# Optimization experiments

Hardware: AMD Instinct MI355X
Metric: run time of the kernel (lower is better)

## Reference

```python
import jax, jax.numpy as jnp
import numpy as np

HEADS, KV_HEADS, HEAD_DIM = 32, 8, 64


def apply_rope(x, cos, sin):
    # x: [b,h,s,d], cos/sin: [s, d//2]; pairs are interleaved (even/odd)
    c = cos[None, None, :, :]
    s = sin[None, None, :, :]
    x1 = x[..., 0::2]
    x2 = x[..., 1::2]
    xn = x1 * c - x2 * s
    yn = x1 * s + x2 * c
    return jnp.stack([xn, yn], axis=-1).reshape(x.shape)


def setup_inputs() -> dict:
    key = jax.random.key(0)
    ks = jax.random.split(key, 7)
    b, s, h = 1, 2048, 2048
    return {
        "x": jax.random.normal(ks[0], (b, s, h), jnp.float32),
        "cos": jax.random.normal(ks[1], (s, HEAD_DIM // 2), jnp.float32),
        "sin": jax.random.normal(ks[2], (s, HEAD_DIM // 2), jnp.float32),
        "Wq": jax.random.normal(ks[3], (h, HEADS * HEAD_DIM), jnp.float32) * 0.02,
        "Wk": jax.random.normal(ks[4], (h, KV_HEADS * HEAD_DIM), jnp.float32) * 0.02,
        "Wv": jax.random.normal(ks[5], (h, KV_HEADS * HEAD_DIM), jnp.float32) * 0.02,
        "Wo": jax.random.normal(ks[6], (HEADS * HEAD_DIM, h), jnp.float32) * 0.02,
    }


def reference(x, cos, sin, Wq, Wk, Wv, Wo):
    b, seq, hidden = x.shape
    Q = x @ Wq  # [b,s,H*d]
    K = x @ Wk  # [b,s,Kh*d]
    V = x @ Wv
    q = Q.reshape(b, seq, HEADS, HEAD_DIM).transpose(0, 2, 1, 3)      # b h s d
    k = K.reshape(b, seq, KV_HEADS, HEAD_DIM).transpose(0, 2, 1, 3)   # b k s d
    v = V.reshape(b, seq, KV_HEADS, HEAD_DIM).transpose(0, 2, 1, 3)
    r = HEADS // KV_HEADS
    # einops 'b k s d -> b (r k) s d': tile kv-head block r times
    k = jnp.tile(k, (1, r, 1, 1))
    v = jnp.tile(v, (1, r, 1, 1))
    q = apply_rope(q, cos, sin)
    k = apply_rope(k, cos, sin)
    scale = 1.0 / jnp.sqrt(jnp.float32(HEAD_DIM))
    qk = jnp.einsum('bhqd,bhkd->bhqk', q, k) * scale
    mask = jnp.triu(jnp.full((seq, seq), -jnp.inf, qk.dtype), k=1)
    attn = jax.nn.softmax(qk + mask, axis=-1)
    av = jnp.einsum('bhqk,bhkd->bhqd', attn, v)
    av = av.transpose(0, 2, 1, 3).reshape(b, seq, HEADS * HEAD_DIM)
    return av @ Wo
```

## Files before the change

### kernel.cpp

```cpp
#include <hip/hip_runtime.h>

typedef unsigned short u16;
typedef __attribute__((ext_vector_type(4))) float f32x4;
typedef __attribute__((ext_vector_type(16))) float f32x16;
typedef __attribute__((ext_vector_type(8))) __bf16 bf16x8;
typedef __attribute__((ext_vector_type(2))) __bf16 bf16x2;

#define HEADS 32
#define KV_HEADS 8
#define HD 64
#define SEQ 2048
#define HID 2048
#define NQK 3072
#define QSCALE (0.125f * 1.4426950408889634f)
#define OCH 2097152u

#define AS1 __attribute__((address_space(1)))
#define AS3 __attribute__((address_space(3)))

__device__ __forceinline__ u16 f2bf(float f) {
  unsigned u = __float_as_uint(f);
  u += 0x7FFFu + ((u >> 16) & 1u);
  return (u16)(u >> 16);
}

__device__ __forceinline__ unsigned pk2(float a, float b) {
  union { bf16x2 h; unsigned u; } c;
  c.h[0] = (__bf16)a; c.h[1] = (__bf16)b;
  return c.u;
}

__device__ __forceinline__ float bflo(unsigned u) {
  return __uint_as_float(u << 16);
}
__device__ __forceinline__ float bfhi(unsigned u) {
  return __uint_as_float(u & 0xFFFF0000u);
}

__device__ __forceinline__ void load16_to_lds(const void* g, void* l) {
  __builtin_amdgcn_global_load_lds((AS1 void*)(void*)g, (AS3 void*)l, 16, 0, 0);
}

__global__ __launch_bounds__(256) void k_f2b(const float* __restrict__ in,
                                             u16* __restrict__ out, int n4) {
  int i = blockIdx.x * 256 + threadIdx.x;
  if (i >= n4) return;
  float4 v = ((const float4*)in)[i];
  ushort4 o;
  o.x = f2bf(v.x); o.y = f2bf(v.y); o.z = f2bf(v.z); o.w = f2bf(v.w);
  ((ushort4*)out)[i] = o;
}

__global__ __launch_bounds__(256) void k_tconv(const float* __restrict__ in, int ldi,
                                               u16* __restrict__ out, int ldo) {
  __shared__ float tile[32][33];
  int c0 = blockIdx.x * 32, r0 = blockIdx.y * 32;
  int col = threadIdx.x & 31, rw = threadIdx.x >> 5;
#pragma unroll
  for (int i = 0; i < 4; i++)
    tile[rw + i * 8][col] = in[(size_t)(r0 + rw + i * 8) * ldi + c0 + col];
  __syncthreads();
#pragma unroll
  for (int i = 0; i < 4; i++)
    out[(size_t)(c0 + rw + i * 8) * ldo + r0 + col] = f2bf(tile[col][rw + i * 8]);
}


__device__ __forceinline__ void stage3(const u16* Asrc, const u16* Bsrc0,
                                       const u16* Bsrc1, u16* AsX, u16* BsX,
                                       int tid) {
  load16_to_lds(Asrc, AsX + tid * 8);
  load16_to_lds(Bsrc0, BsX + tid * 8);
  load16_to_lds(Bsrc1, BsX + 2048 + tid * 8);
}

__device__ __forceinline__ void frag_mfma(const u16* Asb, const u16* Bsb,
                                          const int* aoff, const int* boff,
                                          f32x4 acc[2][4]) {
  bf16x8 a[2], b[4];
#pragma unroll
  for (int i = 0; i < 2; i++)
    a[i] = *(const bf16x8*)((const char*)Asb + aoff[i]);
#pragma unroll
  for (int j = 0; j < 4; j++)
    b[j] = *(const bf16x8*)((const char*)Bsb + boff[j]);
#pragma unroll
  for (int i = 0; i < 2; i++)
#pragma unroll
    for (int j = 0; j < 4; j++)
      acc[i][j] = __builtin_amdgcn_mfma_f32_16x16x32_bf16(a[i], b[j], acc[i][j], 0, 0, 0);
}

__global__ __launch_bounds__(256) void k_gemm(const u16* __restrict__ A,
                                              const u16* __restrict__ Bt,
                                              float* __restrict__ C,
                                              int M, int N, int K) {
  __shared__ u16 As0[64 * 32], As1[64 * 32];
  __shared__ u16 Bs0[128 * 32], Bs1[128 * 32];
  int tid = threadIdx.x;
  int m0 = blockIdx.x * 64, n0 = blockIdx.y * 128;
  int l = tid & 63, w = tid >> 6;
  int lr = l & 15, lg = l >> 4;
  int wr = (w >> 1) * 32, wc = (w & 1) * 64;
  f32x4 acc[2][4] = {};

  int srow = tid >> 2;
  int sseg = (tid & 3) ^ ((srow >> 1) & 3);
  const u16* Asrc = A + (size_t)(m0 + srow) * K + sseg * 8;
  const u16* Bsrc0 = Bt + (size_t)(n0 + srow) * K + sseg * 8;
  const u16* Bsrc1 = Bt + (size_t)(n0 + 64 + srow) * K + sseg * 8;

  int aoff[2], boff[4];
#pragma unroll
  for (int i = 0; i < 2; i++) {
    int r = wr + i * 16 + lr;
    aoff[i] = r * 64 + ((lg ^ ((r >> 1) & 3)) << 4);
  }
#pragma unroll
  for (int j = 0; j < 4; j++) {
    int r = wc + j * 16 + lr;
    boff[j] = r * 64 + ((lg ^ ((r >> 1) & 3)) << 4);
  }

  stage3(Asrc, Bsrc0, Bsrc1, As0, Bs0, tid);
  __syncthreads();
  for (int k0 = 0; k0 < K; k0 += 64) {
    stage3(Asrc + k0 + 32, Bsrc0 + k0 + 32, Bsrc1 + k0 + 32, As1, Bs1, tid);
    frag_mfma(As0, Bs0, aoff, boff, acc);
    __syncthreads();
    if (k0 + 64 < K)
      stage3(Asrc + k0 + 64, Bsrc0 + k0 + 64, Bsrc1 + k0 + 64, As0, Bs0, tid);
    frag_mfma(As1, Bs1, aoff, boff, acc);
    __syncthreads();
  }

#pragma unroll
  for (int i = 0; i < 2; i++)
#pragma unroll
    for (int j = 0; j < 4; j++)
#pragma unroll
      for (int r = 0; r < 4; r++)
        C[(size_t)(m0 + wr + i * 16 + lg * 4 + r) * N + n0 + wc + j * 16 + lr] =
            acc[i][j][r];
}

__global__ __launch_bounds__(256) void k_gemm_qkv(const u16* __restrict__ A,
                                                  const u16* __restrict__ Bt,
                                                  const float* __restrict__ cosp,
                                                  const float* __restrict__ sinp,
                                                  u16* __restrict__ qbuf,
                                                  u16* __restrict__ kbuf,
                                                  u16* __restrict__ vtb) {
  __shared__ u16 As0[64 * 32], As1[64 * 32];
  __shared__ u16 Bs0[128 * 32], Bs1[128 * 32];
  __shared__ u16 Ts[128 * 64];
  const int K = HID;
  int tid = threadIdx.x;
  int m0 = blockIdx.x * 64, n0 = blockIdx.y * 128;
  int l = tid & 63, w = tid >> 6;
  int lr = l & 15, lg = l >> 4;
  int wr = (w >> 1) * 32, wc = (w & 1) * 64;
  f32x4 acc[2][4] = {};

  int srow = tid >> 2;
  int sseg = (tid & 3) ^ ((srow >> 1) & 3);
  const u16* Asrc = A + (size_t)(m0 + srow) * K + sseg * 8;
  const u16* Bsrc0 = Bt + (size_t)(n0 + srow) * K + sseg * 8;
  const u16* Bsrc1 = Bt + (size_t)(n0 + 64 + srow) * K + sseg * 8;

  int aoff[2], boff[4];
#pragma unroll
  for (int i = 0; i < 2; i++) {
    int r = wr + i * 16 + lr;
    aoff[i] = r * 64 + ((lg ^ ((r >> 1) & 3)) << 4);
  }
#pragma unroll
  for (int j = 0; j < 4; j++) {
    int r = wc + j * 16 + lr;
    boff[j] = r * 64 + ((lg ^ ((r >> 1) & 3)) << 4);
  }

  stage3(Asrc, Bsrc0, Bsrc1, As0, Bs0, tid);
  __syncthreads();
  for (int k0 = 0; k0 < K; k0 += 64) {
    stage3(Asrc + k0 + 32, Bsrc0 + k0 + 32, Bsrc1 + k0 + 32, As1, Bs1, tid);
    frag_mfma(As0, Bs0, aoff, boff, acc);
    __syncthreads();
    if (k0 + 64 < K)
      stage3(Asrc + k0 + 64, Bsrc0 + k0 + 64, Bsrc1 + k0 + 64, As0, Bs0, tid);
    frag_mfma(As1, Bs1, aoff, boff, acc);
    __syncthreads();
  }

  if (n0 < 2560) {
    int colbase = n0 + wc;
    bool isQ = colbase < 2048;
    float scale = isQ ? QSCALE : 1.0f;
    u16* base = isQ ? qbuf + (size_t)(colbase >> 6) * SEQ * HD
                    : kbuf + (size_t)((colbase - 2048) >> 6) * SEQ * HD;
    int odd = lr & 1;
#pragma unroll
    for (int i = 0; i < 2; i++)
#pragma unroll
      for (int j = 0; j < 4; j++) {
        int ii = j * 8 + (lr >> 1);
#pragma unroll
        for (int r = 0; r < 4; r++) {
          float v = acc[i][j][r];
          float vp = __shfl_xor(v, 1, 64);
          int sr = m0 + wr + i * 16 + lg * 4 + r;
          float cs = cosp[sr * 32 + ii], sn = sinp[sr * 32 + ii];
          float x1 = odd ? vp : v, x2 = odd ? v : vp;
          float o = odd ? (x1 * sn + x2 * cs) : (x1 * cs - x2 * sn);
          base[(size_t)sr * HD + j * 16 + lr] = f2bf(o * scale);
        }
      }
  } else {
#pragma unroll
    for (int i = 0; i < 2; i++)
#pragma unroll
      for (int j = 0; j < 4; j++)
#pragma unroll
        for (int r = 0; r < 4; r++) {
          int cB = wc + j * 16 + lr, rB = wr + i * 16 + lg * 4 + r;
          *(u16*)((char*)Ts + cB * 128 + ((rB * 2) ^ ((cB & 7) << 4))) =
              f2bf(acc[i][j][r]);
        }
    __syncthreads();
    int c = tid >> 1, half = tid & 1;
    int col = n0 + c;
    int kvh = (col - 2560) >> 6, d = col & 63;
    u16* dst = vtb + (size_t)kvh * HD * SEQ + (size_t)d * SEQ + m0 + half * 32;
    const char* src = (const char*)Ts + c * 128;
    int cs7 = (c & 7) << 4;
#pragma unroll
    for (int q = 0; q < 4; q++)
      *(uint4*)(dst + q * 8) = *(const uint4*)(src + ((half * 64 + q * 16) ^ cs7));
  }
}

__global__ __launch_bounds__(256) void k_flash2(const u16* __restrict__ qb,
                                                const u16* __restrict__ kb,
                                                const u16* __restrict__ vt,
                                                unsigned* __restrict__ Opart,
                                                float2* __restrict__ ml) {
  __shared__ u16 Ks[2][64 * 64];
  __shared__ u16 Vs[2][64 * 64];
  int bid = blockIdx.x;
  int c = bid & 1;
  int b5 = bid >> 1;
  int h = b5 & 31;
  int qi = b5 >> 5;
  int qblk = (SEQ / 128) - 1 - qi;
  int kvh = h & 7;
  int tid = threadIdx.x, w = tid >> 6, l = tid & 63;
  int lq = l & 31, hi = l >> 5;
  const u16* qh = qb + (size_t)h * SEQ * HD;
  const u16* kh = kb + (size_t)kvh * SEQ * HD;
  const u16* vh = vt + (size_t)kvh * HD * SEQ;
  int wq0 = qblk * 128 + w * 32;
  int qg = wq0 + lq;

  bf16x8 qf[4];
#pragma unroll
  for (int ds = 0; ds < 4; ds++)
    qf[ds] = *(const bf16x8*)(qh + (size_t)qg * HD + ds * 16 + hi * 8);

  f32x16 acc[2] = {};
  float m_r = -__builtin_inff(), l_r = 0.f;

  int srow = tid >> 2, c4 = tid & 3, swz = (srow & 7) << 4;
  int sd0 = srow * 128 + ((c4 * 32) ^ swz);
  int sd1 = srow * 128 + ((c4 * 32 + 16) ^ swz);
  const int kt0 = c * (qblk + 1), kt1 = kt0 + qblk + 1;

  {
    const u16* ksrc = kh + (size_t)(kt0 * 64 + srow) * HD + c4 * 16;
    const u16* vsrc = vh + (size_t)srow * SEQ + kt0 * 64 + c4 * 16;
    uint4 a0 = *(const uint4*)(ksrc), a1 = *(const uint4*)(ksrc + 8);
    uint4 b0 = *(const uint4*)(vsrc), b1 = *(const uint4*)(vsrc + 8);
    *(uint4*)((char*)Ks[0] + sd0) = a0; *(uint4*)((char*)Ks[0] + sd1) = a1;
    *(uint4*)((char*)Vs[0] + sd0) = b0; *(uint4*)((char*)Vs[0] + sd1) = b1;
  }
  __syncthreads();

  uint4 kr0, kr1, vr0, vr1;
  int lswz = (lq & 7) << 4;
  for (int kt = kt0; kt < kt1; kt++) {
    int b = (kt - kt0) & 1;
    if (kt + 1 < kt1) {
      const u16* ksrc = kh + (size_t)((kt + 1) * 64 + srow) * HD + c4 * 16;
      const u16* vsrc = vh + (size_t)srow * SEQ + (kt + 1) * 64 + c4 * 16;
      kr0 = *(const uint4*)(ksrc); kr1 = *(const uint4*)(ksrc + 8);
      vr0 = *(const uint4*)(vsrc); vr1 = *(const uint4*)(vsrc + 8);
    }

    if (kt * 64 <= wq0 + 31) {
      f32x16 sT[2] = {};
      const char* kbase = (const char*)Ks[b];
      __builtin_amdgcn_s_setprio(1);
#pragma unroll
      for (int t = 0; t < 2; t++) {
#pragma unroll
        for (int ds = 0; ds < 4; ds++) {
          bf16x8 kf = *(const bf16x8*)(kbase + (t * 32 + lq) * 128 +
                                       ((ds * 32 + hi * 16) ^ lswz));
          sT[t] = __builtin_amdgcn_mfma_f32_32x32x16_bf16(kf, qf[ds], sT[t], 0, 0, 0);
        }
      }
      __builtin_amdgcn_s_setprio(0);

      if (kt * 64 + 63 > wq0) {
#pragma unroll
        for (int t = 0; t < 2; t++)
#pragma unroll
          for (int r = 0; r < 16; r++) {
            int kg = kt * 64 + t * 32 + (r & 3) + 8 * (r >> 2) + 4 * hi;
            if (kg > qg) sT[t][r] = -__builtin_inff();
          }
      }

      float pmax = sT[0][0];
#pragma unroll
      for (int r = 1; r < 16; r++) pmax = fmaxf(pmax, sT[0][r]);
#pragma unroll
      for (int r = 0; r < 16; r++) pmax = fmaxf(pmax, sT[1][r]);
      pmax = fmaxf(pmax, __shfl_xor(pmax, 32, 64));

      if (!__all(pmax <= m_r + 8.f)) {
        float mn = fmaxf(m_r, pmax);
        float scl = __builtin_amdgcn_exp2f(m_r - mn);
        l_r *= scl;
        acc[0] *= scl;
        acc[1] *= scl;
        m_r = mn;
      }

      float ss = 0.f;
#pragma unroll
      for (int t = 0; t < 2; t++)
#pragma unroll
        for (int r = 0; r < 16; r++) {
          float p = __builtin_amdgcn_exp2f(sT[t][r] - m_r);
          sT[t][r] = p;
          ss += p;
        }
      ss += __shfl_xor(ss, 32, 64);
      l_r += ss;

      const char* vbase = (const char*)Vs[b];
#pragma unroll
      for (int t = 0; t < 2; t++) {
        unsigned cp[4][2];
#pragma unroll
        for (int m = 0; m < 4; m++) {
          cp[m][0] = pk2(sT[t][4 * m + 0], sT[t][4 * m + 1]);
          cp[m][1] = pk2(sT[t][4 * m + 2], sT[t][4 * m + 3]);
        }
#pragma unroll
        for (int kl = 0; kl < 2; kl++) {
          unsigned s0 = hi ? cp[2 * kl][0] : cp[2 * kl + 1][0];
          unsigned s1 = hi ? cp[2 * kl][1] : cp[2 * kl + 1][1];
          unsigned r0 = (unsigned)__shfl_xor((int)s0, 32, 64);
          unsigned r1 = (unsigned)__shfl_xor((int)s1, 32, 64);
          union { unsigned u[4]; bf16x8 v; } pa;
          pa.u[0] = hi ? r0 : cp[2 * kl][0];
          pa.u[1] = hi ? r1 : cp[2 * kl][1];
          pa.u[2] = hi ? cp[2 * kl + 1][0] : r0;
          pa.u[3] = hi ? cp[2 * kl + 1][1] : r1;
          int ks = t * 2 + kl;
          __builtin_amdgcn_s_setprio(1);
#pragma unroll
          for (int dt = 0; dt < 2; dt++) {
            bf16x8 vb = *(const bf16x8*)(vbase + (dt * 32 + lq) * 128 +
                                         ((ks * 32 + hi * 16) ^ lswz));
            acc[dt] = __builtin_amdgcn_mfma_f32_32x32x16_bf16(vb, pa.v, acc[dt], 0, 0, 0);
          }
          __builtin_amdgcn_s_setprio(0);
        }
      }
    }

    if (kt + 1 < kt1) {
      *(uint4*)((char*)Ks[b ^ 1] + sd0) = kr0;
      *(uint4*)((char*)Ks[b ^ 1] + sd1) = kr1;
      *(uint4*)((char*)Vs[b ^ 1] + sd0) = vr0;
      *(uint4*)((char*)Vs[b ^ 1] + sd1) = vr1;
    }
    __syncthreads();
  }

  unsigned* op = Opart + (size_t)c * OCH + ((size_t)(b5 * 4 + w) * 16) * 64;
#pragma unroll
  for (int dt = 0; dt < 2; dt++)
#pragma unroll
    for (int j = 0; j < 8; j++)
      op[(dt * 8 + j) * 64 + l] = pk2(acc[dt][2 * j], acc[dt][2 * j + 1]);
  if (!hi)
    ml[c * (HEADS * SEQ) + h * SEQ + wq0 + lq] = make_float2(m_r, l_r);
}

__global__ __launch_bounds__(256) void k_merge(const unsigned* __restrict__ Opart,
                                               const float2* __restrict__ ml,
                                               u16* __restrict__ av) {
  __shared__ u16 Ts[8192];
  int bid = blockIdx.x;
  int h = bid & 31, qblk = bid >> 5;
  int b5 = ((SEQ / 128 - 1 - qblk) << 5) | h;
  int tid = threadIdx.x, w = tid >> 6, l = tid & 63;
  int lq = l & 31, hi = l >> 5;
  int wq0 = qblk * 128 + w * 32;

  float2 ml0 = ml[h * SEQ + wq0 + lq];
  float2 ml1 = ml[HEADS * SEQ + h * SEQ + wq0 + lq];
  float m = fmaxf(ml0.x, ml1.x);
  float f0 = __builtin_amdgcn_exp2f(ml0.x - m);
  float f1 = __builtin_amdgcn_exp2f(ml1.x - m);
  float inv = 1.0f / (ml0.y * f0 + ml1.y * f1);

  const unsigned* op0 = Opart + ((size_t)(b5 * 4 + w) * 16) * 64;
  const unsigned* op1 = op0 + OCH;
  f32x16 acc[2];
#pragma unroll
  for (int dt = 0; dt < 2; dt++)
#pragma unroll
    for (int j = 0; j < 8; j++) {
      unsigned a0 = op0[(dt * 8 + j) * 64 + l];
      unsigned a1 = op1[(dt * 8 + j) * 64 + l];
      acc[dt][2 * j] = bflo(a0) * f0 + bflo(a1) * f1;
      acc[dt][2 * j + 1] = bfhi(a0) * f0 + bfhi(a1) * f1;
    }

  int lswz = (lq & 7) << 4;
  char* wbase = (char*)Ts + w * 4096;
#pragma unroll
  for (int dt = 0; dt < 2; dt++)
#pragma unroll
    for (int m4 = 0; m4 < 4; m4++) {
      int r0 = 4 * m4;
      uint2 pr;
      pr.x = pk2(acc[dt][r0 + 0] * inv, acc[dt][r0 + 1] * inv);
      pr.y = pk2(acc[dt][r0 + 2] * inv, acc[dt][r0 + 3] * inv);
      int byte = lq * 128 + ((dt * 64 + m4 * 16 + hi * 8) ^ lswz);
      *(uint2*)(wbase + byte) = pr;
    }
  __syncthreads();
  int q2 = l >> 1, cH = l & 1;
  int qswz = (q2 & 7) << 4;
#pragma unroll
  for (int i = 0; i < 4; i++) {
    uint4 d = *(const uint4*)(wbase + q2 * 128 + ((cH * 64 + i * 16) ^ qswz));
    *(uint4*)(av + (size_t)(wq0 + q2) * HID + h * HD + cH * 32 + i * 8) = d;
  }
}

extern "C" void kernel_launch(void* const* d_in, const int* in_sizes, int n_in,
                              void* d_out, int out_size, void* d_ws, size_t ws_size,
                              hipStream_t stream) {
  (void)in_sizes; (void)n_in; (void)out_size; (void)ws_size;
  const float* x = (const float*)d_in[0];
  const float* cosp = (const float*)d_in[1];
  const float* sinp = (const float*)d_in[2];
  const float* Wq = (const float*)d_in[3];
  const float* Wk = (const float*)d_in[4];
  const float* Wv = (const float*)d_in[5];
  const float* Wo = (const float*)d_in[6];
  float* out = (float*)d_out;
  char* ws = (char*)d_ws;

  u16* xb = (u16*)(ws);
  float2* mlb = (float2*)(ws);
  u16* Wqkv = (u16*)(ws + ((size_t)8 << 20));
  u16* WoT = (u16*)(ws + ((size_t)20 << 20));
  u16* qbuf = (u16*)(ws + ((size_t)28 << 20));
  u16* kbuf = (u16*)(ws + ((size_t)36 << 20));
  u16* vtb = (u16*)(ws + ((size_t)38 << 20));
  u16* av = (u16*)(ws + ((size_t)40 << 20));
  unsigned* Opart = (unsigned*)(ws + ((size_t)48 << 20));

  k_f2b<<<(SEQ * HID / 4 + 255) / 256, 256, 0, stream>>>(x, xb, SEQ * HID / 4);
  k_tconv<<<dim3(HID / 32, HID / 32), 256, 0, stream>>>(Wq, HID, Wqkv, HID);
  k_tconv<<<dim3(512 / 32, HID / 32), 256, 0, stream>>>(Wk, 512, Wqkv + (size_t)2048 * HID, HID);
  k_tconv<<<dim3(512 / 32, HID / 32), 256, 0, stream>>>(Wv, 512, Wqkv + (size_t)2560 * HID, HID);
  k_tconv<<<dim3(HID / 32, HID / 32), 256, 0, stream>>>(Wo, HID, WoT, HID);
  k_gemm_qkv<<<dim3(SEQ / 64, NQK / 128), 256, 0, stream>>>(xb, Wqkv, cosp, sinp,
                                                            qbuf, kbuf, vtb);
  k_flash2<<<(SEQ / 128) * HEADS * 2, 256, 0, stream>>>(qbuf, kbuf, vtb, Opart, mlb);
  k_merge<<<(SEQ / 128) * HEADS, 256, 0, stream>>>(Opart, mlb, av);
  k_gemm<<<dim3(SEQ / 64, HID / 128), 256, 0, stream>>>(av, WoT, out, SEQ, HID, HID);
}
```

Measured before the change: 141.3 us.

## Triple-buffer GEMM LDS staging with vmcnt-based waits and fewer barriers

```diff
diff --git a/kernel.cpp b/kernel.cpp
--- a/kernel.cpp
+++ b/kernel.cpp
@@ -68,10 +68,10 @@
 
 __device__ __forceinline__ void stage3(const u16* Asrc, const u16* Bsrc0,
                                        const u16* Bsrc1, u16* AsX, u16* BsX,
-                                       int tid) {
-  load16_to_lds(Asrc, AsX + tid * 8);
-  load16_to_lds(Bsrc0, BsX + tid * 8);
-  load16_to_lds(Bsrc1, BsX + 2048 + tid * 8);
+                                       int tid, int koff) {
+  load16_to_lds(Asrc + koff, AsX + tid * 8);
+  load16_to_lds(Bsrc0 + koff, BsX + tid * 8);
+  load16_to_lds(Bsrc1 + koff, BsX + 2048 + tid * 8);
 }
 
 __device__ __forceinline__ void frag_mfma(const u16* Asb, const u16* Bsb,
@@ -91,12 +91,32 @@
       acc[i][j] = __builtin_amdgcn_mfma_f32_16x16x32_bf16(a[i], b[j], acc[i][j], 0, 0, 0);
 }
 
+#define TILE_STEP(AsX, BsX, tnext)                              \
+  do {                                                          \
+    asm volatile("s_waitcnt vmcnt(6)" ::: "memory");            \
+    __builtin_amdgcn_sched_barrier(0);                          \
+    __builtin_amdgcn_s_barrier();                               \
+    frag_mfma(AsX, BsX, aoff, boff, acc);                       \
+    __builtin_amdgcn_sched_barrier(0);                          \
+    __builtin_amdgcn_s_barrier();                               \
+    stage3(Asrc, Bsrc0, Bsrc1, AsX, BsX, tid, (tnext) * 32);    \
+  } while (0)
+
+#define TILE_TAIL(AsX, BsX, n)                                  \
+  do {                                                          \
+    asm volatile("s_waitcnt vmcnt(" #n ")" ::: "memory");       \
+    __builtin_amdgcn_sched_barrier(0);                          \
+    __builtin_amdgcn_s_barrier();                               \
+    frag_mfma(AsX, BsX, aoff, boff, acc);                       \
+  } while (0)
+
 __global__ __launch_bounds__(256) void k_gemm(const u16* __restrict__ A,
                                               const u16* __restrict__ Bt,
                                               float* __restrict__ C,
                                               int M, int N, int K) {
-  __shared__ u16 As0[64 * 32], As1[64 * 32];
-  __shared__ u16 Bs0[128 * 32], Bs1[128 * 32];
+  __shared__ u16 smem[18432];
+  u16* As0 = smem;          u16* As1 = smem + 2048;  u16* As2 = smem + 4096;
+  u16* Bs0 = smem + 6144;   u16* Bs1 = smem + 10240; u16* Bs2 = smem + 14336;
   int tid = threadIdx.x;
   int m0 = blockIdx.x * 64, n0 = blockIdx.y * 128;
   int l = tid & 63, w = tid >> 6;
@@ -122,17 +142,19 @@
     boff[j] = r * 64 + ((lg ^ ((r >> 1) & 3)) << 4);
   }
 
-  stage3(Asrc, Bsrc0, Bsrc1, As0, Bs0, tid);
-  __syncthreads();
-  for (int k0 = 0; k0 < K; k0 += 64) {
-    stage3(Asrc + k0 + 32, Bsrc0 + k0 + 32, Bsrc1 + k0 + 32, As1, Bs1, tid);
-    frag_mfma(As0, Bs0, aoff, boff, acc);
-    __syncthreads();
-    if (k0 + 64 < K)
-      stage3(Asrc + k0 + 64, Bsrc0 + k0 + 64, Bsrc1 + k0 + 64, As0, Bs0, tid);
-    frag_mfma(As1, Bs1, aoff, boff, acc);
-    __syncthreads();
-  }
+  stage3(Asrc, Bsrc0, Bsrc1, As0, Bs0, tid, 0);
+  stage3(Asrc, Bsrc0, Bsrc1, As1, Bs1, tid, 32);
+  stage3(Asrc, Bsrc0, Bsrc1, As2, Bs2, tid, 64);
+#pragma unroll 1
+  for (int t = 0; t < 60; t += 3) {
+    TILE_STEP(As0, Bs0, t + 3);
+    TILE_STEP(As1, Bs1, t + 4);
+    TILE_STEP(As2, Bs2, t + 5);
+  }
+  TILE_STEP(As0, Bs0, 63);
+  TILE_TAIL(As1, Bs1, 6);
+  TILE_TAIL(As2, Bs2, 3);
+  TILE_TAIL(As0, Bs0, 0);
 
 #pragma unroll
   for (int i = 0; i < 2; i++)
@@ -151,9 +173,10 @@
                                                   u16* __restrict__ qbuf,
                                                   u16* __restrict__ kbuf,
                                                   u16* __restrict__ vtb) {
-  __shared__ u16 As0[64 * 32], As1[64 * 32];
-  __shared__ u16 Bs0[128 * 32], Bs1[128 * 32];
-  __shared__ u16 Ts[128 * 64];
+  __shared__ u16 smem[18432];
+  u16* As0 = smem;          u16* As1 = smem + 2048;  u16* As2 = smem + 4096;
+  u16* Bs0 = smem + 6144;   u16* Bs1 = smem + 10240; u16* Bs2 = smem + 14336;
+  u16* Ts = smem;
   const int K = HID;
   int tid = threadIdx.x;
   int m0 = blockIdx.x * 64, n0 = blockIdx.y * 128;
@@ -180,17 +203,19 @@
     boff[j] = r * 64 + ((lg ^ ((r >> 1) & 3)) << 4);
   }
 
-  stage3(Asrc, Bsrc0, Bsrc1, As0, Bs0, tid);
-  __syncthreads();
-  for (int k0 = 0; k0 < K; k0 += 64) {
-    stage3(Asrc + k0 + 32, Bsrc0 + k0 + 32, Bsrc1 + k0 + 32, As1, Bs1, tid);
-    frag_mfma(As0, Bs0, aoff, boff, acc);
-    __syncthreads();
-    if (k0 + 64 < K)
-      stage3(Asrc + k0 + 64, Bsrc0 + k0 + 64, Bsrc1 + k0 + 64, As0, Bs0, tid);
-    frag_mfma(As1, Bs1, aoff, boff, acc);
-    __syncthreads();
-  }
+  stage3(Asrc, Bsrc0, Bsrc1, As0, Bs0, tid, 0);
+  stage3(Asrc, Bsrc0, Bsrc1, As1, Bs1, tid, 32);
+  stage3(Asrc, Bsrc0, Bsrc1, As2, Bs2, tid, 64);
+#pragma unroll 1
+  for (int t = 0; t < 60; t += 3) {
+    TILE_STEP(As0, Bs0, t + 3);
+    TILE_STEP(As1, Bs1, t + 4);
+    TILE_STEP(As2, Bs2, t + 5);
+  }
+  TILE_STEP(As0, Bs0, 63);
+  TILE_TAIL(As1, Bs1, 6);
+  TILE_TAIL(As2, Bs2, 3);
+  TILE_TAIL(As0, Bs0, 0);
 
   if (n0 < 2560) {
     int colbase = n0 + wc;
@@ -216,6 +241,7 @@
         }
       }
   } else {
+    __syncthreads();
 #pragma unroll
     for (int i = 0; i < 2; i++)
 #pragma unroll
```

Result: faster. 138.4 us (-2.0%).
